# Kernel optimization log

Hardware: AMD Instinct MI355X
Metric: run time of the kernel (lower is better)

Reference implementation:

```python
import jax, jax.numpy as jnp
import numpy as np

HINGE_VALUE = 1.0

def setup_inputs() -> dict:
    key = jax.random.key(0)
    k1, k2 = jax.random.split(key)
    x_pred = jax.random.normal(k1, (8192, 128), dtype=jnp.float32)
    x_target = jax.random.normal(k2, (16384, 128), dtype=jnp.float32)
    return {"x_pred": x_pred, "x_target": x_target, "top_k": 5}


def _cdist(a, b):
    # Euclidean distance via GEMM form: ||a||^2 + ||b||^2 - 2 a.b
    a2 = jnp.sum(a * a, axis=-1, keepdims=True)          # [N,1]
    b2 = jnp.sum(b * b, axis=-1, keepdims=True).T        # [1,M]
    d2 = a2 + b2 - 2.0 * (a @ b.T)                       # [N,M]
    return jnp.sqrt(jnp.maximum(d2, 0.0))


def reference(x_pred, x_target, top_k):
    c_dist = _cdist(x_pred, x_target)                    # [N,M]
    # smallest-k distances per pred point
    neg_vals, _ = jax.lax.top_k(-c_dist, top_k)          # [N,k]
    values = jnp.maximum(-neg_vals - HINGE_VALUE, 0.0)   # hinge
    return jnp.mean(values)
```

## Files before the change

kernel.cpp:

```cpp
#include <hip/hip_runtime.h>
#include <hip/hip_bf16.h>
#include <float.h>

#define N_PRED 8192
#define M_TGT  16384
#define KD     128
#define TOPK   5
#define SPLITS 16
#define MSPLIT (M_TGT / SPLITS)
#define TILE_T 128
#define NTILES (MSPLIT / TILE_T)
#define ROWS_PER_BLOCK 256
#define ROWBLKS (N_PRED / ROWS_PER_BLOCK)

using short8  = __attribute__((ext_vector_type(8))) short;
using floatx4 = __attribute__((ext_vector_type(4))) float;

__device__ __forceinline__ unsigned short f2bf(float v) {
    unsigned int u = __float_as_uint(v);
    u = (u + 0x7FFFu + ((u >> 16) & 1u)) >> 16;
    return (unsigned short)u;
}

__device__ __forceinline__ void async16(const void* g, void* l) {
    __builtin_amdgcn_global_load_lds(
        (const __attribute__((address_space(1))) unsigned int*)g,
        (__attribute__((address_space(3))) unsigned int*)l, 16, 0, 0);
}
__device__ __forceinline__ void async4(const void* g, void* l) {
    __builtin_amdgcn_global_load_lds(
        (const __attribute__((address_space(1))) unsigned int*)g,
        (__attribute__((address_space(3))) unsigned int*)l, 4, 0, 0);
}

__device__ __forceinline__ void ins5(float* t, float d) {
    t[4] = __builtin_amdgcn_fmed3f(d, t[3], t[4]);
    t[3] = __builtin_amdgcn_fmed3f(d, t[2], t[3]);
    t[2] = __builtin_amdgcn_fmed3f(d, t[1], t[2]);
    t[1] = __builtin_amdgcn_fmed3f(d, t[0], t[1]);
    t[0] = fminf(t[0], d);
}

__global__ void prep_kernel(const float* __restrict__ pred,
                            const float* __restrict__ tgt,
                            unsigned short* __restrict__ predB,
                            unsigned short* __restrict__ tgtB,
                            float* __restrict__ a2,
                            float* __restrict__ b2,
                            float* __restrict__ acc,
                            unsigned int* __restrict__ counter) {
    const int row = blockIdx.x * 8 + (threadIdx.x >> 5);
    const int l32 = threadIdx.x & 31;
    const float* src;
    unsigned short* dst;
    float scale;
    float* norm;
    if (row < N_PRED) {
        src = pred + (size_t)row * KD;
        dst = predB + (size_t)row * KD;
        scale = -2.0f;
        norm = a2 + row;
    } else {
        const int rr = row - N_PRED;
        src = tgt + (size_t)rr * KD;
        dst = tgtB + (size_t)rr * KD;
        scale = 1.0f;
        norm = b2 + rr;
    }
    const float4 x = reinterpret_cast<const float4*>(src)[l32];
    uint2 p;
    p.x = (unsigned int)f2bf(x.x * scale) | ((unsigned int)f2bf(x.y * scale) << 16);
    p.y = (unsigned int)f2bf(x.z * scale) | ((unsigned int)f2bf(x.w * scale) << 16);
    reinterpret_cast<uint2*>(dst)[l32] = p;
    float s = x.x * x.x + x.y * x.y + x.z * x.z + x.w * x.w;
    #pragma unroll
    for (int off = 16; off > 0; off >>= 1) s += __shfl_down(s, off, 32);
    if (l32 == 0) norm[0] = s;
    if (blockIdx.x == 0 && threadIdx.x == 0) { acc[0] = 0.0f; counter[0] = 0u; }
}

__global__ __launch_bounds__(512, 4) void density_kernel(
        const unsigned short* __restrict__ predB,
        const unsigned short* __restrict__ tgtB,
        const float* __restrict__ b2,
        float* __restrict__ wsTop) {
    const int tid   = threadIdx.x;
    const int wave  = tid >> 6;
    const int lane  = tid & 63;
    const int col   = lane & 15;
    const int quad  = lane >> 4;
    const int split = blockIdx.x & (SPLITS - 1);
    const int rowblk = blockIdx.x >> 4;
    const int r0 = rowblk * ROWS_PER_BLOCK + wave * 32;
    const int m0 = split * MSPLIT;

    __shared__ short8 frag[2][TILE_T * 16];
    __shared__ float  b2s[2][TILE_T];

    short8 afrag[2][4];
    #pragma unroll
    for (int rf = 0; rf < 2; rf++)
        #pragma unroll
        for (int kf = 0; kf < 4; kf++)
            afrag[rf][kf] = *reinterpret_cast<const short8*>(
                predB + (size_t)(r0 + rf * 16 + col) * KD + kf * 32 + quad * 8);

    float t5[2][4][5];
    #pragma unroll
    for (int rf = 0; rf < 2; rf++)
        #pragma unroll
        for (int rg = 0; rg < 4; rg++)
            #pragma unroll
            for (int j = 0; j < 5; j++)
                t5[rf][rg][j] = FLT_MAX;

    {
        #pragma unroll
        for (int s = 0; s < 4; ++s) {
            const int ci = wave * 4 + s, g = ci >> 2, kf = ci & 3;
            const unsigned short* src =
                tgtB + (size_t)(m0 + g * 16 + col) * KD + kf * 32 + quad * 8;
            async16(src, &frag[0][ci * 64]);
        }
        if (wave < 2) async4(b2 + m0 + wave * 64 + lane, &b2s[0][wave * 64]);
    }
    __syncthreads();

    for (int t = 0; t < NTILES; ++t) {
        const int cur = t & 1;
        if (t + 1 < NTILES) {
            const int m0t = m0 + (t + 1) * TILE_T;
            #pragma unroll
            for (int s = 0; s < 4; ++s) {
                const int ci = wave * 4 + s, g = ci >> 2, kf = ci & 3;
                const unsigned short* src =
                    tgtB + (size_t)(m0t + g * 16 + col) * KD + kf * 32 + quad * 8;
                async16(src, &frag[cur ^ 1][ci * 64]);
            }
            if (wave < 2) async4(b2 + m0t + wave * 64 + lane, &b2s[cur ^ 1][wave * 64]);
        }

        #pragma unroll
        for (int g = 0; g < 8; ++g) {
            const float bq = b2s[cur][g * 16 + col];
            short8 bf[4];
            #pragma unroll
            for (int kf = 0; kf < 4; ++kf)
                bf[kf] = frag[cur][(g * 4 + kf) * 64 + lane];
            #pragma unroll
            for (int rf = 0; rf < 2; ++rf) {
                floatx4 c = {bq, bq, bq, bq};
                c = __builtin_amdgcn_mfma_f32_16x16x32_bf16(afrag[rf][0], bf[0], c, 0, 0, 0);
                c = __builtin_amdgcn_mfma_f32_16x16x32_bf16(afrag[rf][1], bf[1], c, 0, 0, 0);
                c = __builtin_amdgcn_mfma_f32_16x16x32_bf16(afrag[rf][2], bf[2], c, 0, 0, 0);
                c = __builtin_amdgcn_mfma_f32_16x16x32_bf16(afrag[rf][3], bf[3], c, 0, 0, 0);
                #pragma unroll
                for (int rg = 0; rg < 4; ++rg) ins5(t5[rf][rg], c[rg]);
            }
        }
        __syncthreads();
    }

    #pragma unroll
    for (int off = 1; off < 16; off <<= 1) {
        #pragma unroll
        for (int rf = 0; rf < 2; ++rf)
            #pragma unroll
            for (int rg = 0; rg < 4; ++rg) {
                float o0 = __shfl_xor(t5[rf][rg][0], off);
                float o1 = __shfl_xor(t5[rf][rg][1], off);
                float o2 = __shfl_xor(t5[rf][rg][2], off);
                float o3 = __shfl_xor(t5[rf][rg][3], off);
                float o4 = __shfl_xor(t5[rf][rg][4], off);
                ins5(t5[rf][rg], o0); ins5(t5[rf][rg], o1); ins5(t5[rf][rg], o2);
                ins5(t5[rf][rg], o3); ins5(t5[rf][rg], o4);
            }
    }

    if (col == 0) {
        #pragma unroll
        for (int rf = 0; rf < 2; ++rf)
            #pragma unroll
            for (int rg = 0; rg < 4; ++rg) {
                const int row = r0 + rf * 16 + quad * 4 + rg;
                float* dst = wsTop + ((size_t)row * SPLITS + split) * 5;
                #pragma unroll
                for (int j = 0; j < 5; ++j) dst[j] = t5[rf][rg][j];
            }
    }
}

__global__ void merge_kernel(const float* __restrict__ wsTop,
                             const float* __restrict__ a2,
                             float* __restrict__ acc,
                             unsigned int* __restrict__ counter,
                             float* __restrict__ out) {
    const int row = blockIdx.x * 256 + threadIdx.x;
    const float* p = wsTop + (size_t)row * (SPLITS * 5);
    float u[5] = {FLT_MAX, FLT_MAX, FLT_MAX, FLT_MAX, FLT_MAX};
    #pragma unroll
    for (int i = 0; i < SPLITS * 5; ++i) ins5(u, p[i]);
    const float a = a2[row];
    float hs = 0.0f;
    #pragma unroll
    for (int j = 0; j < 5; ++j) {
        const float dd = sqrtf(fmaxf(u[j] + a, 0.0f));
        hs += fmaxf(dd - 1.0f, 0.0f);
    }
    #pragma unroll
    for (int off = 32; off > 0; off >>= 1) hs += __shfl_down(hs, off);
    __shared__ float ws[4];
    if ((threadIdx.x & 63) == 0) ws[threadIdx.x >> 6] = hs;
    __syncthreads();
    if (threadIdx.x == 0) {
        atomicAdd(acc, ws[0] + ws[1] + ws[2] + ws[3]);
        __threadfence();
        const unsigned int done = atomicAdd(counter, 1u);
        if (done == gridDim.x - 1) {
            const float tot = atomicAdd(acc, 0.0f);
            out[0] = tot * (1.0f / (float)(N_PRED * TOPK));
        }
    }
}

extern "C" void kernel_launch(void* const* d_in, const int* in_sizes, int n_in,
                              void* d_out, int out_size, void* d_ws, size_t ws_size,
                              hipStream_t stream) {
    const float* pred = (const float*)d_in[0];
    const float* tgt  = (const float*)d_in[1];
    char* ws = (char*)d_ws;
    unsigned short* predB = (unsigned short*)(ws);
    unsigned short* tgtB  = (unsigned short*)(ws + (size_t)2 * 1024 * 1024);
    float* a2   = (float*)(ws + (size_t)6 * 1024 * 1024);
    float* b2   = (float*)(ws + (size_t)6 * 1024 * 1024 + 32 * 1024);
    float* acc  = (float*)(ws + (size_t)6 * 1024 * 1024 + 96 * 1024);
    unsigned int* counter = (unsigned int*)(ws + (size_t)6 * 1024 * 1024 + 96 * 1024 + 64);
    float* wsTop = (float*)(ws + (size_t)6 * 1024 * 1024 + 128 * 1024);
    float* out = (float*)d_out;

    prep_kernel<<<(N_PRED + M_TGT) / 8, 256, 0, stream>>>(pred, tgt, predB, tgtB, a2, b2, acc, counter);
    density_kernel<<<ROWBLKS * SPLITS, 512, 0, stream>>>(predB, tgtB, b2, wsTop);
    merge_kernel<<<N_PRED / 256, 256, 0, stream>>>(wsTop, a2, acc, counter, out);
}
```

Measured before the change: 127.8 us.

## Track per-lane top-2 in main loop and recompute overflowing buckets in finalize

```diff
diff --git a/kernel.cpp b/kernel.cpp
--- a/kernel.cpp
+++ b/kernel.cpp
@@ -12,6 +12,7 @@
 #define NTILES (MSPLIT / TILE_T)
 #define ROWS_PER_BLOCK 256
 #define ROWBLKS (N_PRED / ROWS_PER_BLOCK)
+#define NBLKROW (SPLITS * 16)
 
 using short8  = __attribute__((ext_vector_type(8))) short;
 using floatx4 = __attribute__((ext_vector_type(4))) float;
@@ -39,6 +40,26 @@
     t[2] = __builtin_amdgcn_fmed3f(d, t[1], t[2]);
     t[1] = __builtin_amdgcn_fmed3f(d, t[0], t[1]);
     t[0] = fminf(t[0], d);
+}
+
+__device__ __forceinline__ void bmerge(float* u) {
+    #pragma unroll
+    for (int off = 1; off < 64; off <<= 1) {
+        float o0 = __shfl_xor(u[0], off);
+        float o1 = __shfl_xor(u[1], off);
+        float o2 = __shfl_xor(u[2], off);
+        float o3 = __shfl_xor(u[3], off);
+        float o4 = __shfl_xor(u[4], off);
+        ins5(u, o0); ins5(u, o1); ins5(u, o2); ins5(u, o3); ins5(u, o4);
+    }
+}
+
+__device__ __forceinline__ float dotd(unsigned int p, unsigned int t) {
+    const float plo = __uint_as_float(p << 16);
+    const float phi = __uint_as_float(p & 0xFFFF0000u);
+    const float tlo = __uint_as_float(t << 16);
+    const float thi = __uint_as_float(t & 0xFFFF0000u);
+    return plo * tlo + phi * thi;
 }
 
 __global__ void prep_kernel(const float* __restrict__ pred,
@@ -83,7 +104,7 @@
         const unsigned short* __restrict__ predB,
         const unsigned short* __restrict__ tgtB,
         const float* __restrict__ b2,
-        float* __restrict__ wsTop) {
+        float2* __restrict__ wsMin) {
     const int tid   = threadIdx.x;
     const int wave  = tid >> 6;
     const int lane  = tid & 63;
@@ -105,14 +126,12 @@
             afrag[rf][kf] = *reinterpret_cast<const short8*>(
                 predB + (size_t)(r0 + rf * 16 + col) * KD + kf * 32 + quad * 8);
 
-    float t5[2][4][5];
+    float2 bm[2][4];
     #pragma unroll
     for (int rf = 0; rf < 2; rf++)
         #pragma unroll
         for (int rg = 0; rg < 4; rg++)
-            #pragma unroll
-            for (int j = 0; j < 5; j++)
-                t5[rf][rg][j] = FLT_MAX;
+            bm[rf][rg] = make_float2(FLT_MAX, FLT_MAX);
 
     {
         #pragma unroll
@@ -147,78 +166,119 @@
             #pragma unroll
             for (int kf = 0; kf < 4; ++kf)
                 bf[kf] = frag[cur][(g * 4 + kf) * 64 + lane];
+            const floatx4 ci = {bq, bq, bq, bq};
             #pragma unroll
             for (int rf = 0; rf < 2; ++rf) {
-                floatx4 c = {bq, bq, bq, bq};
-                c = __builtin_amdgcn_mfma_f32_16x16x32_bf16(afrag[rf][0], bf[0], c, 0, 0, 0);
+                floatx4 c;
+                c = __builtin_amdgcn_mfma_f32_16x16x32_bf16(afrag[rf][0], bf[0], ci, 0, 0, 0);
                 c = __builtin_amdgcn_mfma_f32_16x16x32_bf16(afrag[rf][1], bf[1], c, 0, 0, 0);
                 c = __builtin_amdgcn_mfma_f32_16x16x32_bf16(afrag[rf][2], bf[2], c, 0, 0, 0);
                 c = __builtin_amdgcn_mfma_f32_16x16x32_bf16(afrag[rf][3], bf[3], c, 0, 0, 0);
                 #pragma unroll
-                for (int rg = 0; rg < 4; ++rg) ins5(t5[rf][rg], c[rg]);
+                for (int rg = 0; rg < 4; ++rg) {
+                    const float d = c[rg];
+                    bm[rf][rg].y = __builtin_amdgcn_fmed3f(d, bm[rf][rg].x, bm[rf][rg].y);
+                    bm[rf][rg].x = fminf(bm[rf][rg].x, d);
+                }
             }
         }
         __syncthreads();
     }
 
     #pragma unroll
-    for (int off = 1; off < 16; off <<= 1) {
-        #pragma unroll
-        for (int rf = 0; rf < 2; ++rf)
-            #pragma unroll
-            for (int rg = 0; rg < 4; ++rg) {
-                float o0 = __shfl_xor(t5[rf][rg][0], off);
-                float o1 = __shfl_xor(t5[rf][rg][1], off);
-                float o2 = __shfl_xor(t5[rf][rg][2], off);
-                float o3 = __shfl_xor(t5[rf][rg][3], off);
-                float o4 = __shfl_xor(t5[rf][rg][4], off);
-                ins5(t5[rf][rg], o0); ins5(t5[rf][rg], o1); ins5(t5[rf][rg], o2);
-                ins5(t5[rf][rg], o3); ins5(t5[rf][rg], o4);
+    for (int rf = 0; rf < 2; ++rf)
+        #pragma unroll
+        for (int rg = 0; rg < 4; ++rg) {
+            const int row = r0 + rf * 16 + quad * 4 + rg;
+            wsMin[((size_t)row * SPLITS + split) * 16 + col] = bm[rf][rg];
+        }
+}
+
+__global__ __launch_bounds__(512) void finalize_kernel(
+        const float2* __restrict__ wsMin,
+        const unsigned short* __restrict__ predB,
+        const unsigned short* __restrict__ tgtB,
+        const float* __restrict__ b2,
+        const float* __restrict__ a2,
+        float* __restrict__ acc,
+        unsigned int* __restrict__ counter,
+        float* __restrict__ out) {
+    const int wave = threadIdx.x >> 6;
+    const int lane = threadIdx.x & 63;
+    const int row  = blockIdx.x * 8 + wave;
+
+    const float2* pv = wsMin + (size_t)row * NBLKROW + lane * 4;
+    float2 v[4];
+    #pragma unroll
+    for (int j = 0; j < 4; ++j) v[j] = pv[j];
+
+    float u[5] = {FLT_MAX, FLT_MAX, FLT_MAX, FLT_MAX, FLT_MAX};
+    #pragma unroll
+    for (int j = 0; j < 4; ++j) { ins5(u, v[j].x); ins5(u, v[j].y); }
+    bmerge(u);
+    const float m5 = u[4];
+
+    unsigned long long fl[4];
+    #pragma unroll
+    for (int j = 0; j < 4; ++j) fl[j] = __ballot(v[j].y <= m5);
+
+    if (fl[0] | fl[1] | fl[2] | fl[3]) {
+        #pragma unroll
+        for (int j = 0; j < 4; ++j)
+            if (v[j].y <= m5) { v[j].x = FLT_MAX; v[j].y = FLT_MAX; }
+        #pragma unroll
+        for (int j = 0; j < 5; ++j) u[j] = FLT_MAX;
+        #pragma unroll
+        for (int j = 0; j < 4; ++j) { ins5(u, v[j].x); ins5(u, v[j].y); }
+        bmerge(u);
+        #pragma unroll
+        for (int j = 0; j < 4; ++j) {
+            unsigned long long m = fl[j];
+            while (m) {
+                const int bit = __ffsll((unsigned long long)m) - 1;
+                m &= m - 1;
+                const int blk = bit * 4 + j;
+                const int sp = blk >> 4, cb = blk & 15;
+                const int tg = sp * MSPLIT + lane * 16 + cb;
+                float s = b2[tg];
+                const uint4* tp = reinterpret_cast<const uint4*>(tgtB + (size_t)tg * KD);
+                const uint4* pp = reinterpret_cast<const uint4*>(predB + (size_t)row * KD);
+                #pragma unroll
+                for (int i = 0; i < 16; ++i) {
+                    const uint4 pa = pp[i], tb = tp[i];
+                    s += dotd(pa.x, tb.x) + dotd(pa.y, tb.y)
+                       + dotd(pa.z, tb.z) + dotd(pa.w, tb.w);
+                }
+                float w[5] = {s, FLT_MAX, FLT_MAX, FLT_MAX, FLT_MAX};
+                bmerge(w);
+                #pragma unroll
+                for (int q = 0; q < 5; ++q) ins5(u, w[q]);
             }
-    }
-
-    if (col == 0) {
-        #pragma unroll
-        for (int rf = 0; rf < 2; ++rf)
-            #pragma unroll
-            for (int rg = 0; rg < 4; ++rg) {
-                const int row = r0 + rf * 16 + quad * 4 + rg;
-                float* dst = wsTop + ((size_t)row * SPLITS + split) * 5;
-                #pragma unroll
-                for (int j = 0; j < 5; ++j) dst[j] = t5[rf][rg][j];
-            }
-    }
-}
-
-__global__ void merge_kernel(const float* __restrict__ wsTop,
-                             const float* __restrict__ a2,
-                             float* __restrict__ acc,
-                             unsigned int* __restrict__ counter,
-                             float* __restrict__ out) {
-    const int row = blockIdx.x * 256 + threadIdx.x;
-    const float* p = wsTop + (size_t)row * (SPLITS * 5);
-    float u[5] = {FLT_MAX, FLT_MAX, FLT_MAX, FLT_MAX, FLT_MAX};
-    #pragma unroll
-    for (int i = 0; i < SPLITS * 5; ++i) ins5(u, p[i]);
-    const float a = a2[row];
-    float hs = 0.0f;
-    #pragma unroll
-    for (int j = 0; j < 5; ++j) {
-        const float dd = sqrtf(fmaxf(u[j] + a, 0.0f));
-        hs += fmaxf(dd - 1.0f, 0.0f);
-    }
-    #pragma unroll
-    for (int off = 32; off > 0; off >>= 1) hs += __shfl_down(hs, off);
-    __shared__ float ws[4];
-    if ((threadIdx.x & 63) == 0) ws[threadIdx.x >> 6] = hs;
+        }
+    }
+
+    __shared__ float hsum[8];
+    if (lane == 0) {
+        const float a = a2[row];
+        float hs = 0.0f;
+        #pragma unroll
+        for (int j = 0; j < 5; ++j) {
+            const float dd = sqrtf(fmaxf(u[j] + a, 0.0f));
+            hs += fmaxf(dd - 1.0f, 0.0f);
+        }
+        hsum[wave] = hs;
+    }
     __syncthreads();
     if (threadIdx.x == 0) {
-        atomicAdd(acc, ws[0] + ws[1] + ws[2] + ws[3]);
+        float tot = 0.0f;
+        #pragma unroll
+        for (int w = 0; w < 8; ++w) tot += hsum[w];
+        atomicAdd(acc, tot);
         __threadfence();
         const unsigned int done = atomicAdd(counter, 1u);
         if (done == gridDim.x - 1) {
-            const float tot = atomicAdd(acc, 0.0f);
-            out[0] = tot * (1.0f / (float)(N_PRED * TOPK));
+            const float t = atomicAdd(acc, 0.0f);
+            out[0] = t * (1.0f / (float)(N_PRED * TOPK));
         }
     }
 }
@@ -235,10 +295,10 @@
     float* b2   = (float*)(ws + (size_t)6 * 1024 * 1024 + 32 * 1024);
     float* acc  = (float*)(ws + (size_t)6 * 1024 * 1024 + 96 * 1024);
     unsigned int* counter = (unsigned int*)(ws + (size_t)6 * 1024 * 1024 + 96 * 1024 + 64);
-    float* wsTop = (float*)(ws + (size_t)6 * 1024 * 1024 + 128 * 1024);
+    float2* wsMin = (float2*)(ws + (size_t)6 * 1024 * 1024 + 128 * 1024);
     float* out = (float*)d_out;
 
     prep_kernel<<<(N_PRED + M_TGT) / 8, 256, 0, stream>>>(pred, tgt, predB, tgtB, a2, b2, acc, counter);
-    density_kernel<<<ROWBLKS * SPLITS, 512, 0, stream>>>(predB, tgtB, b2, wsTop);
-    merge_kernel<<<N_PRED / 256, 256, 0, stream>>>(wsTop, a2, acc, counter, out);
-}
+    density_kernel<<<ROWBLKS * SPLITS, 512, 0, stream>>>(predB, tgtB, b2, wsMin);
+    finalize_kernel<<<N_PRED / 8, 512, 0, stream>>>(wsMin, predB, tgtB, b2, a2, acc, counter, out);
+}
```

New measurement: 144.7 us. 1.13x slower.
